# Optimization experiments

Hardware: AMD Instinct MI355X
Metric: run time of the kernel (lower is better)

The kernel has to match this reference:

```python
import jax, jax.numpy as jnp
import numpy as np

DIM = 32          # d_model == channel dim of the volume
D_STATE = 16
D_CONV = 4
EXPAND = 2
D_INNER = EXPAND * DIM        # 64
DT_RANK = max(1, (DIM + 15) // 16)  # ceil(d_model/16) = 2
LN_EPS = 1e-5


def setup_inputs() -> dict:
    key = jax.random.key(0)
    ks = jax.random.split(key, 12)
    B, Dd, Hh, Ww = 1, 32, 32, 32
    sc = 0.02
    x = jax.random.normal(ks[0], (B, DIM, Dd, Hh, Ww), jnp.float32)
    ln_w = jnp.ones((DIM,), jnp.float32)
    ln_b = jnp.zeros((DIM,), jnp.float32)
    in_proj_w = jax.random.normal(ks[1], (2 * D_INNER, DIM), jnp.float32) * sc
    conv_w = jax.random.normal(ks[2], (D_INNER, 1, D_CONV), jnp.float32) * sc
    conv_b = jnp.zeros((D_INNER,), jnp.float32)
    x_proj_w = jax.random.normal(ks[3], (DT_RANK + 2 * D_STATE, D_INNER), jnp.float32) * sc
    dt_proj_w = jax.random.normal(ks[4], (D_INNER, DT_RANK), jnp.float32) * sc
    dt_proj_b = jax.random.uniform(ks[5], (D_INNER,), jnp.float32, -4.0, -2.0)  # small softplus(dt) at init
    # Mamba S4D-real init: A = -[1..d_state], stored as A_log
    A_log = jnp.log(jnp.broadcast_to(jnp.arange(1, D_STATE + 1, dtype=jnp.float32), (D_INNER, D_STATE)))
    D_param = jnp.ones((D_INNER,), jnp.float32)
    out_proj_w = jax.random.normal(ks[6], (DIM, D_INNER), jnp.float32) * sc
    return {
        "x": x, "ln_w": ln_w, "ln_b": ln_b, "in_proj_w": in_proj_w,
        "conv_w": conv_w, "conv_b": conv_b, "x_proj_w": x_proj_w,
        "dt_proj_w": dt_proj_w, "dt_proj_b": dt_proj_b, "A_log": A_log,
        "D_param": D_param, "out_proj_w": out_proj_w,
    }


def _mamba_layer(x, ln_w, ln_b, in_proj_w, conv_w, conv_b, x_proj_w,
                 dt_proj_w, dt_proj_b, A_log, D_param, out_proj_w):
    B, C, Dd, Hh, Ww = x.shape
    L = Dd * Hh * Ww
    # z-scan flatten: (B, C, D, H, W) -> (B, L, C)
    xf = x.reshape(B, C, L).transpose(0, 2, 1)
    # LayerNorm over channel dim
    mu = jnp.mean(xf, axis=-1, keepdims=True)
    var = jnp.mean(jnp.square(xf - mu), axis=-1, keepdims=True)
    xn = (xf - mu) * jax.lax.rsqrt(var + LN_EPS) * ln_w + ln_b
    # in_proj -> x, z branches
    xz = xn @ in_proj_w.T                      # (B, L, 2*d_inner)
    x_in, z = jnp.split(xz, 2, axis=-1)
    # depthwise causal conv1d over sequence
    xt = x_in.transpose(0, 2, 1)               # (B, d_inner, L)
    xc = jax.lax.conv_general_dilated(
        xt, conv_w, window_strides=(1,), padding=[(D_CONV - 1, 0)],
        feature_group_count=D_INNER)
    xc = jax.nn.silu(xc + conv_b[None, :, None]).transpose(0, 2, 1)  # (B, L, d_inner)
    # input-dependent dt, B, C
    x_dbl = xc @ x_proj_w.T                    # (B, L, dt_rank + 2*d_state)
    dt, Bm, Cm = jnp.split(x_dbl, [DT_RANK, DT_RANK + D_STATE], axis=-1)
    delta = jax.nn.softplus(dt @ dt_proj_w.T + dt_proj_b)            # (B, L, d_inner)
    A = -jnp.exp(A_log)                        # (d_inner, d_state)
    # discretize: h_t = exp(delta*A) h_{t-1} + delta*B_t*x_t
    dA = jnp.exp(delta[..., None] * A)                               # (B, L, d_inner, d_state)
    dBx = delta[..., None] * Bm[:, :, None, :] * xc[..., None]       # (B, L, d_inner, d_state)
    def comb(e1, e2):
        a1, b1 = e1
        a2, b2 = e2
        return (a1 * a2, a2 * b1 + b2)
    _, h = jax.lax.associative_scan(comb, (dA, dBx), axis=1)         # parallel linear recurrence
    y = jnp.einsum('blds,bls->bld', h, Cm) + xc * D_param            # (B, L, d_inner)
    y = y * jax.nn.silu(z)
    out = y @ out_proj_w.T                     # (B, L, C)
    # unpermute z-scan
    return out.transpose(0, 2, 1).reshape(B, C, Dd, Hh, Ww)


def reference(x, ln_w, ln_b, in_proj_w, conv_w, conv_b, x_proj_w,
              dt_proj_w, dt_proj_b, A_log, D_param, out_proj_w):
    return _mamba_layer(x, ln_w, ln_b, in_proj_w, conv_w, conv_b, x_proj_w,
                        dt_proj_w, dt_proj_b, A_log, D_param, out_proj_w)
```

## Files before the change

### kernel.cpp

```cpp
#include <hip/hip_runtime.h>
#include <hip/hip_bf16.h>

constexpr int L   = 32768;
constexpr int CD  = 32;
constexpr int DI  = 64;
constexpr int DS  = 16;
constexpr int LC  = 64;
constexpr int NCH = L / LC;
constexpr int NPAIR = DI * DS;

constexpr size_t FL        = (size_t)DI * L;
constexpr size_t OFF_SZ    = 0;
constexpr size_t OFF_XC    = FL;
constexpr size_t OFF_DELTA = 2 * FL;
constexpr size_t OFF_BM    = 3 * FL;
constexpr size_t OFF_CM    = OFF_BM + (size_t)DS * L;
constexpr size_t OFF_APROD = OFF_CM + (size_t)DS * L;
constexpr size_t OFF_CARRY = OFF_APROD;
constexpr size_t OFF_BACC  = OFF_APROD + (size_t)NCH * NPAIR;

__device__ __forceinline__ float bf2f(__hip_bfloat16 v) { return __bfloat162float(v); }
__device__ __forceinline__ void f4arr(const float4 v, float* a) { a[0]=v.x; a[1]=v.y; a[2]=v.z; a[3]=v.w; }

__device__ __forceinline__ bool detect_bf16(const void* ln_w) {
    return ((const unsigned short*)ln_w)[0] == 0x3F80;
}
__device__ __forceinline__ float ldin(const void* p, size_t i, bool bf16) {
    return bf16 ? bf2f(((const __hip_bfloat16*)p)[i]) : ((const float*)p)[i];
}

__global__ __launch_bounds__(256) void k12_featurize_scan(
    const void* __restrict__ x,
    const void* __restrict__ ln_w,
    const void* __restrict__ ln_b,
    const void* __restrict__ in_proj_w,
    const void* __restrict__ conv_w,
    const void* __restrict__ conv_b,
    const void* __restrict__ x_proj_w,
    const void* __restrict__ dt_proj_w,
    const void* __restrict__ dt_proj_b,
    const void* __restrict__ A_log,
    float* __restrict__ ws)
{
    __shared__ __align__(16) char smem[67840];
    float (*xin_s)[69]  = (float(*)[69])(smem);
    char* AR = smem + 17664;
    float (*xn_s)[33]   = (float(*)[33])(AR);
    float (*w_in_s)[32] = (float(*)[32])(AR + 8848);
    float (*sdl)[68]    = (float(*)[68])(AR);
    float (*sxc)[68]    = (float(*)[68])(AR + 17408);
    float (*sbm)[68]    = (float(*)[68])(AR + 34816);
    char* FW = smem + 56832;
    float (*w_xp)[64]   = (float(*)[64])(FW);
    float (*w_cv)[4]    = (float(*)[4])(FW + 8704);
    float (*w_dt)[2]    = (float(*)[2])(FW + 9728);
    float* b_dt_s = (float*)(FW + 10240);
    float* b_cv_s = (float*)(FW + 10496);
    float* lnw_s  = (float*)(FW + 10752);
    float* lnb_s  = (float*)(FW + 10880);

    const int tid = threadIdx.x;
    const int l0  = blockIdx.x * LC;
    const bool isb = detect_bf16(ln_w);

    if (isb) {
        const __hip_bfloat16* ipw = (const __hip_bfloat16*)in_proj_w;
        const __hip_bfloat16* xpw = (const __hip_bfloat16*)x_proj_w;
        for (int i = tid; i < 128 * 32; i += 256) w_in_s[i >> 5][i & 31] = bf2f(ipw[i]);
        for (int i = tid; i < 34 * 64; i += 256)  w_xp[i >> 6][i & 63] = bf2f(xpw[i]);
    } else {
        const float* ipw = (const float*)in_proj_w;
        const float* xpw = (const float*)x_proj_w;
        for (int i = tid; i < 128 * 32; i += 256) w_in_s[i >> 5][i & 31] = ipw[i];
        for (int i = tid; i < 34 * 64; i += 256)  w_xp[i >> 6][i & 63] = xpw[i];
    }
    w_cv[tid >> 2][tid & 3] = ldin(conv_w, tid, isb);
    if (tid < 128) w_dt[tid >> 1][tid & 1] = ldin(dt_proj_w, tid, isb);
    if (tid < 64) { b_dt_s[tid] = ldin(dt_proj_b, tid, isb); b_cv_s[tid] = ldin(conv_b, tid, isb); }
    if (tid < 32) { lnw_s[tid] = ldin(ln_w, tid, isb); lnb_s[tid] = ldin(ln_b, tid, isb); }
    __syncthreads();

    if (tid < LC + 3) {
        const int l = l0 - 3 + tid;
        const bool valid = (l >= 0);
        const int lc = valid ? l : 0;
        float xv[CD];
        if (isb) {
            const __hip_bfloat16* xb = (const __hip_bfloat16*)x;
            #pragma unroll
            for (int c = 0; c < CD; ++c) xv[c] = bf2f(xb[(size_t)c * L + lc]);
        } else {
            const float* xf = (const float*)x;
            #pragma unroll
            for (int c = 0; c < CD; ++c) xv[c] = xf[(size_t)c * L + lc];
        }
        float mu = 0.f;
        #pragma unroll
        for (int c = 0; c < CD; ++c) mu += xv[c];
        mu *= (1.f / CD);
        float var = 0.f;
        #pragma unroll
        for (int c = 0; c < CD; ++c) { const float dc = xv[c] - mu; var += dc * dc; }
        const float rstd = rsqrtf(var * (1.f / CD) + 1e-5f);
        #pragma unroll
        for (int c = 0; c < CD; ++c)
            xn_s[tid][c] = valid ? ((xv[c] - mu) * rstd * lnw_s[c] + lnb_s[c]) : 0.f;
    }
    __syncthreads();

    {
        const int wv   = tid >> 6;
        const int lane = tid & 63;
        const int jb   = wv * 32;
        if (wv < 2) {
            const int pos1  = 64 + lane;
            const bool v1   = (pos1 < LC + 3);
            const int pos1c = v1 ? pos1 : 66;
            float xv0[CD], xv1[CD];
            #pragma unroll
            for (int c = 0; c < CD; ++c) { xv0[c] = xn_s[lane][c]; xv1[c] = xn_s[pos1c][c]; }
            for (int j = 0; j < 32; ++j) {
                const float4* wr = (const float4*)w_in_s[jb + j];
                float a0 = 0.f, a1 = 0.f;
                #pragma unroll
                for (int q = 0; q < 8; ++q) {
                    const float4 w4 = wr[q];
                    a0 += w4.x * xv0[4*q] + w4.y * xv0[4*q+1] + w4.z * xv0[4*q+2] + w4.w * xv0[4*q+3];
                    a1 += w4.x * xv1[4*q] + w4.y * xv1[4*q+1] + w4.z * xv1[4*q+2] + w4.w * xv1[4*q+3];
                }
                xin_s[jb + j][lane] = a0;
                if (v1) xin_s[jb + j][pos1] = a1;
            }
        } else {
            const int l = l0 + lane;
            float xv[CD];
            #pragma unroll
            for (int c = 0; c < CD; ++c) xv[c] = xn_s[3 + lane][c];
            for (int j = 0; j < 32; ++j) {
                const float4* wr = (const float4*)w_in_s[jb + j];
                float acc = 0.f;
                #pragma unroll
                for (int q = 0; q < 8; ++q) {
                    const float4 w4 = wr[q];
                    acc += w4.x * xv[4*q] + w4.y * xv[4*q+1] + w4.z * xv[4*q+2] + w4.w * xv[4*q+3];
                }
                const float s = acc / (1.f + __expf(-acc));
                ws[OFF_SZ + (size_t)(jb - 64 + j) * L + l] = s;
            }
        }
    }
    __syncthreads();

    {
        const int h  = tid & 3;
        const int pq = tid >> 2;
        const int l  = l0 + pq;
        const int dbase = h * 16;
        float xcv[16];
        #pragma unroll
        for (int i = 0; i < 16; ++i) {
            const int d = dbase + i;
            float acc = b_cv_s[d];
            #pragma unroll
            for (int k = 0; k < 4; ++k) acc += w_cv[d][k] * xin_s[d][pq + k];
            const float v = acc / (1.f + __expf(-acc));
            xcv[i] = v;
            ws[OFF_XC + (size_t)d * L + l] = v;
            sxc[d][pq] = v;
        }
        float dt0 = 0.f, dt1 = 0.f;
        for (int r = 0; r < 34; ++r) {
            float acc = 0.f;
            #pragma unroll
            for (int i = 0; i < 16; ++i) acc += w_xp[r][dbase + i] * xcv[i];
            acc += __shfl_xor(acc, 1);
            acc += __shfl_xor(acc, 2);
            if (r == 0) dt0 = acc;
            else if (r == 1) dt1 = acc;
            else {
                const int rr = r - 2;
                if (h == (rr >> 3)) {
                    const size_t off = (rr < 16) ? (OFF_BM + (size_t)rr * L)
                                                 : (OFF_CM + (size_t)(rr - 16) * L);
                    ws[off + l] = acc;
                    if (rr < 16) sbm[rr][pq] = acc;
                }
            }
        }
        #pragma unroll
        for (int i = 0; i < 16; ++i) {
            const int d = dbase + i;
            const float tv = dt0 * w_dt[d][0] + dt1 * w_dt[d][1] + b_dt_s[d];
            const float sp = fmaxf(tv, 0.f) + log1pf(__expf(-fabsf(tv)));
            ws[OFF_DELTA + (size_t)d * L + l] = sp;
            sdl[d][pq] = sp;
        }
    }
    __syncthreads();

    {
        const int d = tid >> 2, sg = tid & 3;
        float Aj[4], ap[4] = {1.f, 1.f, 1.f, 1.f}, bb[4] = {0.f, 0.f, 0.f, 0.f};
        #pragma unroll
        for (int j = 0; j < 4; ++j) Aj[j] = -__expf(ldin(A_log, d * DS + sg + 4 * j, isb));

        for (int t = 0; t < LC; t += 4) {
            float ddv[4], xxv[4], bm[4][4];
            f4arr(*(const float4*)&sdl[d][t], ddv);
            f4arr(*(const float4*)&sxc[d][t], xxv);
            f4arr(*(const float4*)&sbm[sg][t],      bm[0]);
            f4arr(*(const float4*)&sbm[sg + 4][t],  bm[1]);
            f4arr(*(const float4*)&sbm[sg + 8][t],  bm[2]);
            f4arr(*(const float4*)&sbm[sg + 12][t], bm[3]);
            #pragma unroll
            for (int tt = 0; tt < 4; ++tt) {
                const float dxc = ddv[tt] * xxv[tt];
                #pragma unroll
                for (int j = 0; j < 4; ++j) {
                    const float e = __expf(ddv[tt] * Aj[j]);
                    ap[j] *= e;
                    bb[j] = e * bb[j] + dxc * bm[j][tt];
                }
            }
        }
        #pragma unroll
        for (int j = 0; j < 4; ++j) {
            const size_t p = (size_t)(tid * 4 + j);
            ws[OFF_APROD + p * NCH + blockIdx.x] = ap[j];
            ws[OFF_BACC  + p * NCH + blockIdx.x] = bb[j];
        }
    }
}

__global__ __launch_bounds__(256) void k3_carry(float* __restrict__ ws)
{
    const int lane = threadIdx.x & 63;
    const int p    = blockIdx.x * 4 + (threadIdx.x >> 6);
    const size_t row_a = OFF_APROD + (size_t)p * NCH;
    const size_t row_b = OFF_BACC  + (size_t)p * NCH;

    float a[8], b[8];
    f4arr(*(const float4*)&ws[row_a + lane * 8],     a);
    f4arr(*(const float4*)&ws[row_a + lane * 8 + 4], a + 4);
    f4arr(*(const float4*)&ws[row_b + lane * 8],     b);
    f4arr(*(const float4*)&ws[row_b + lane * 8 + 4], b + 4);

    float Ag = a[0], Bg = b[0];
    #pragma unroll
    for (int i = 1; i < 8; ++i) { Bg = a[i] * Bg + b[i]; Ag = Ag * a[i]; }
    #pragma unroll
    for (int off = 1; off < 64; off <<= 1) {
        const float pa = __shfl_up(Ag, off);
        const float pb = __shfl_up(Bg, off);
        if (lane >= off) { Bg = Ag * pb + Bg; Ag = Ag * pa; }
    }
    float Pb = __shfl_up(Bg, 1);
    if (lane == 0) Pb = 0.f;
    float cr[8];
    #pragma unroll
    for (int i = 0; i < 8; ++i) { cr[i] = Pb; Pb = a[i] * Pb + b[i]; }
    *(float4*)&ws[OFF_CARRY + (size_t)p * NCH + lane * 8]     = make_float4(cr[0], cr[1], cr[2], cr[3]);
    *(float4*)&ws[OFF_CARRY + (size_t)p * NCH + lane * 8 + 4] = make_float4(cr[4], cr[5], cr[6], cr[7]);
}

__global__ __launch_bounds__(256, 3) void k45_apply_out(
    const void* __restrict__ A_log,
    const void* __restrict__ D_param,
    const void* __restrict__ ln_w,
    const void* __restrict__ out_proj_w,
    float* __restrict__ ws,
    void* __restrict__ out)
{
    __shared__ __align__(16) float sbm[DS][68];
    __shared__ __align__(16) float scm[DS][68];
    __shared__ __align__(16) float sy[DI][68];
    __shared__ float w_out_s[CD][DI];
    const int tid = threadIdx.x;
    const int c   = blockIdx.x;
    const size_t t0 = (size_t)c * LC;
    const bool isb = detect_bf16(ln_w);

    if (isb) {
        const __hip_bfloat16* opw = (const __hip_bfloat16*)out_proj_w;
        for (int i = tid; i < CD * DI; i += 256) w_out_s[i >> 6][i & 63] = bf2f(opw[i]);
    } else {
        const float* opw = (const float*)out_proj_w;
        for (int i = tid; i < CD * DI; i += 256) w_out_s[i >> 6][i & 63] = opw[i];
    }
    {
        const int r = tid >> 4, t4 = (tid & 15) * 4;
        *(float4*)&sbm[r][t4] = *(const float4*)&ws[OFF_BM + (size_t)r * L + t0 + t4];
        *(float4*)&scm[r][t4] = *(const float4*)&ws[OFF_CM + (size_t)r * L + t0 + t4];
    }

    const int d = tid >> 2, sg = tid & 3;
    float Aj[4];
    #pragma unroll
    for (int j = 0; j < 4; ++j) Aj[j] = -__expf(ldin(A_log, d * DS + sg + 4 * j, isb));
    const float Dd = ldin(D_param, d, isb);
    float hh[4];
    #pragma unroll
    for (int j = 0; j < 4; ++j) hh[j] = ws[OFF_CARRY + (size_t)(tid * 4 + j) * NCH + c];
    __syncthreads();

    const float* dlp = ws + OFF_DELTA + (size_t)d * L + t0;
    const float* xcp = ws + OFF_XC    + (size_t)d * L + t0;
    float4 dd4 = *(const float4*)dlp;
    float4 xx4 = *(const float4*)xcp;
    for (int t = 0; t < LC; t += 4) {
        const int tn = (t + 4) & 63;
        const float4 ddn = *(const float4*)(dlp + tn);
        const float4 xxn = *(const float4*)(xcp + tn);
        float ddv[4], xxv[4], bm[4][4], cm[4][4];
        f4arr(dd4, ddv);
        f4arr(xx4, xxv);
        f4arr(*(const float4*)&sbm[sg][t],      bm[0]);
        f4arr(*(const float4*)&sbm[sg + 4][t],  bm[1]);
        f4arr(*(const float4*)&sbm[sg + 8][t],  bm[2]);
        f4arr(*(const float4*)&sbm[sg + 12][t], bm[3]);
        f4arr(*(const float4*)&scm[sg][t],      cm[0]);
        f4arr(*(const float4*)&scm[sg + 4][t],  cm[1]);
        f4arr(*(const float4*)&scm[sg + 8][t],  cm[2]);
        f4arr(*(const float4*)&scm[sg + 12][t], cm[3]);
        #pragma unroll
        for (int tt = 0; tt < 4; ++tt) {
            const float dxc = ddv[tt] * xxv[tt];
            float ys = 0.f;
            #pragma unroll
            for (int j = 0; j < 4; ++j) {
                const float e = __expf(ddv[tt] * Aj[j]);
                hh[j] = e * hh[j] + dxc * bm[j][tt];
                ys += hh[j] * cm[j][tt];
            }
            ys += __shfl_xor(ys, 1);
            ys += __shfl_xor(ys, 2);
            if (sg == 0) sy[d][t + tt] = ys + xxv[tt] * Dd;
        }
        dd4 = ddn; xx4 = xxn;
    }
    __syncthreads();

    #pragma unroll
    for (int k = 0; k < 4; ++k) {
        const int idx = tid + k * 256;
        const int r = idx >> 4, t4 = (idx & 15) * 4;
        float4 yv = *(float4*)&sy[r][t4];
        const float4 zv = *(const float4*)&ws[OFF_SZ + (size_t)r * L + t0 + t4];
        yv.x *= zv.x; yv.y *= zv.y; yv.z *= zv.z; yv.w *= zv.w;
        *(float4*)&sy[r][t4] = yv;
    }
    __syncthreads();

    {
        const int wv   = tid >> 6;
        const int lane = tid & 63;
        float acc[8] = {0.f, 0.f, 0.f, 0.f, 0.f, 0.f, 0.f, 0.f};
        for (int dd = 0; dd < DI; ++dd) {
            const float yv = sy[dd][lane];
            #pragma unroll
            for (int j = 0; j < 8; ++j)
                acc[j] += yv * w_out_s[wv * 8 + j][dd];
        }
        const size_t l = t0 + lane;
        #pragma unroll
        for (int j = 0; j < 8; ++j) {
            const int cc = wv * 8 + j;
            if (isb) ((__hip_bfloat16*)out)[(size_t)cc * L + l] = __float2bfloat16(acc[j]);
            else     ((float*)out)[(size_t)cc * L + l] = acc[j];
        }
    }
}

extern "C" void kernel_launch(void* const* d_in, const int* in_sizes, int n_in,
                              void* d_out, int out_size, void* d_ws, size_t ws_size,
                              hipStream_t stream)
{
    (void)in_sizes; (void)n_in; (void)out_size; (void)ws_size;
    const void* x        = d_in[0];
    const void* ln_w     = d_in[1];
    const void* ln_b     = d_in[2];
    const void* in_pw    = d_in[3];
    const void* conv_w   = d_in[4];
    const void* conv_b   = d_in[5];
    const void* x_pw     = d_in[6];
    const void* dt_pw    = d_in[7];
    const void* dt_pb    = d_in[8];
    const void* A_log    = d_in[9];
    const void* D_param  = d_in[10];
    const void* out_pw   = d_in[11];
    float* ws = (float*)d_ws;

    k12_featurize_scan<<<NCH, 256, 0, stream>>>(x, ln_w, ln_b, in_pw, conv_w, conv_b,
                                                x_pw, dt_pw, dt_pb, A_log, ws);
    k3_carry<<<NPAIR / 4, 256, 0, stream>>>(ws);
    k45_apply_out<<<NCH, 256, 0, stream>>>(A_log, D_param, ln_w, out_pw, ws, d_out);
}
```

Baseline: 162.0 us.

## Fuse three-kernel Mamba pipeline into one cooperative kernel with grid syncs

```diff
diff --git a/kernel.cpp b/kernel.cpp
--- a/kernel.cpp
+++ b/kernel.cpp
@@ -1,5 +1,8 @@
 #include <hip/hip_runtime.h>
 #include <hip/hip_bf16.h>
+#include <hip/hip_cooperative_groups.h>
+
+namespace cg = cooperative_groups;
 
 constexpr int L   = 32768;
 constexpr int CD  = 32;
@@ -8,6 +11,10 @@
 constexpr int LC  = 64;
 constexpr int NCH = L / LC;
 constexpr int NPAIR = DI * DS;
+
+constexpr size_t COFF_A = 0;
+constexpr size_t COFF_B = (size_t)NCH * NPAIR;
+constexpr size_t COFF_C = 2 * (size_t)NCH * NPAIR;
 
 constexpr size_t FL        = (size_t)DI * L;
 constexpr size_t OFF_SZ    = 0;
@@ -27,6 +34,316 @@
 }
 __device__ __forceinline__ float ldin(const void* p, size_t i, bool bf16) {
     return bf16 ? bf2f(((const __hip_bfloat16*)p)[i]) : ((const float*)p)[i];
+}
+
+__global__ __launch_bounds__(256, 2) void mamba_fused(
+    const void* __restrict__ x,
+    const void* __restrict__ ln_w,
+    const void* __restrict__ ln_b,
+    const void* __restrict__ in_proj_w,
+    const void* __restrict__ conv_w,
+    const void* __restrict__ conv_b,
+    const void* __restrict__ x_proj_w,
+    const void* __restrict__ dt_proj_w,
+    const void* __restrict__ dt_proj_b,
+    const void* __restrict__ A_log,
+    const void* __restrict__ D_param,
+    const void* __restrict__ out_proj_w,
+    float* __restrict__ ws,
+    void* __restrict__ out)
+{
+    __shared__ __align__(16) char smem[72192];
+    float (*xin_s)[69]  = (float(*)[69])(smem);
+    float (*ctile)[512] = (float(*)[512])(smem);
+    float (*sy)[68]     = (float(*)[68])(smem);
+    char* AR = smem + 17664;
+    float (*xn_s)[33]   = (float(*)[33])(AR);
+    float (*w_in_s)[32] = (float(*)[32])(AR + 8848);
+    float (*sdl)[68]    = (float(*)[68])(AR);
+    float (*sxc)[68]    = (float(*)[68])(AR + 17408);
+    float (*sbm)[68]    = (float(*)[68])(AR + 34816);
+    float (*scm)[68]    = (float(*)[68])(AR + 39168);
+    char* FW = smem + 61184;
+    float (*w_xp)[64]   = (float(*)[64])(FW);
+    float (*w_out_s)[64]= (float(*)[64])(FW);
+    float (*w_cv)[4]    = (float(*)[4])(FW + 8704);
+    float (*w_dt)[2]    = (float(*)[2])(FW + 9728);
+    float* b_dt_s = (float*)(FW + 10240);
+    float* b_cv_s = (float*)(FW + 10496);
+    float* lnw_s  = (float*)(FW + 10752);
+    float* lnb_s  = (float*)(FW + 10880);
+
+    cg::grid_group grid = cg::this_grid();
+
+    const int tid  = threadIdx.x;
+    const int c    = blockIdx.x;
+    const int l0   = c * LC;
+    const int wv   = tid >> 6;
+    const int lane = tid & 63;
+    const bool isb = detect_bf16(ln_w);
+
+    float szr[32];
+    float Aj[4];
+
+    if (isb) {
+        const __hip_bfloat16* ipw = (const __hip_bfloat16*)in_proj_w;
+        const __hip_bfloat16* xpw = (const __hip_bfloat16*)x_proj_w;
+        for (int i = tid; i < 128 * 32; i += 256) w_in_s[i >> 5][i & 31] = bf2f(ipw[i]);
+        for (int i = tid; i < 34 * 64; i += 256)  w_xp[i >> 6][i & 63] = bf2f(xpw[i]);
+    } else {
+        const float* ipw = (const float*)in_proj_w;
+        const float* xpw = (const float*)x_proj_w;
+        for (int i = tid; i < 128 * 32; i += 256) w_in_s[i >> 5][i & 31] = ipw[i];
+        for (int i = tid; i < 34 * 64; i += 256)  w_xp[i >> 6][i & 63] = xpw[i];
+    }
+    w_cv[tid >> 2][tid & 3] = ldin(conv_w, tid, isb);
+    if (tid < 128) w_dt[tid >> 1][tid & 1] = ldin(dt_proj_w, tid, isb);
+    if (tid < 64) { b_dt_s[tid] = ldin(dt_proj_b, tid, isb); b_cv_s[tid] = ldin(conv_b, tid, isb); }
+    if (tid < 32) { lnw_s[tid] = ldin(ln_w, tid, isb); lnb_s[tid] = ldin(ln_b, tid, isb); }
+    __syncthreads();
+
+    if (tid < LC + 3) {
+        const int l = l0 - 3 + tid;
+        const bool valid = (l >= 0);
+        const int lc = valid ? l : 0;
+        float xv[CD];
+        if (isb) {
+            const __hip_bfloat16* xb = (const __hip_bfloat16*)x;
+            #pragma unroll
+            for (int ch = 0; ch < CD; ++ch) xv[ch] = bf2f(xb[(size_t)ch * L + lc]);
+        } else {
+            const float* xf = (const float*)x;
+            #pragma unroll
+            for (int ch = 0; ch < CD; ++ch) xv[ch] = xf[(size_t)ch * L + lc];
+        }
+        float mu = 0.f;
+        #pragma unroll
+        for (int ch = 0; ch < CD; ++ch) mu += xv[ch];
+        mu *= (1.f / CD);
+        float var = 0.f;
+        #pragma unroll
+        for (int ch = 0; ch < CD; ++ch) { const float dc = xv[ch] - mu; var += dc * dc; }
+        const float rstd = rsqrtf(var * (1.f / CD) + 1e-5f);
+        #pragma unroll
+        for (int ch = 0; ch < CD; ++ch)
+            xn_s[tid][ch] = valid ? ((xv[ch] - mu) * rstd * lnw_s[ch] + lnb_s[ch]) : 0.f;
+    }
+    __syncthreads();
+
+    if (wv < 2) {
+        const int jb = wv * 32;
+        const int pos1  = 64 + lane;
+        const bool v1   = (pos1 < LC + 3);
+        const int pos1c = v1 ? pos1 : 66;
+        float xv0[CD], xv1[CD];
+        #pragma unroll
+        for (int ch = 0; ch < CD; ++ch) { xv0[ch] = xn_s[lane][ch]; xv1[ch] = xn_s[pos1c][ch]; }
+        for (int j = 0; j < 32; ++j) {
+            const float4* wr = (const float4*)w_in_s[jb + j];
+            float a0 = 0.f, a1 = 0.f;
+            #pragma unroll
+            for (int q = 0; q < 8; ++q) {
+                const float4 w4 = wr[q];
+                a0 += w4.x * xv0[4*q] + w4.y * xv0[4*q+1] + w4.z * xv0[4*q+2] + w4.w * xv0[4*q+3];
+                a1 += w4.x * xv1[4*q] + w4.y * xv1[4*q+1] + w4.z * xv1[4*q+2] + w4.w * xv1[4*q+3];
+            }
+            xin_s[jb + j][lane] = a0;
+            if (v1) xin_s[jb + j][pos1] = a1;
+        }
+    } else {
+        const int jb = wv * 32;
+        float xv[CD];
+        #pragma unroll
+        for (int ch = 0; ch < CD; ++ch) xv[ch] = xn_s[3 + lane][ch];
+        #pragma unroll
+        for (int j = 0; j < 32; ++j) {
+            const float4* wr = (const float4*)w_in_s[jb + j];
+            float acc = 0.f;
+            #pragma unroll
+            for (int q = 0; q < 8; ++q) {
+                const float4 w4 = wr[q];
+                acc += w4.x * xv[4*q] + w4.y * xv[4*q+1] + w4.z * xv[4*q+2] + w4.w * xv[4*q+3];
+            }
+            szr[j] = acc / (1.f + __expf(-acc));
+        }
+    }
+    __syncthreads();
+
+    {
+        const int h  = tid & 3;
+        const int pq = tid >> 2;
+        const int dbase = h * 16;
+        float xcv[16];
+        #pragma unroll
+        for (int i = 0; i < 16; ++i) {
+            const int d = dbase + i;
+            float acc = b_cv_s[d];
+            #pragma unroll
+            for (int k = 0; k < 4; ++k) acc += w_cv[d][k] * xin_s[d][pq + k];
+            const float v = acc / (1.f + __expf(-acc));
+            xcv[i] = v;
+            sxc[d][pq] = v;
+        }
+        float dt0 = 0.f, dt1 = 0.f;
+        for (int r = 0; r < 34; ++r) {
+            float acc = 0.f;
+            #pragma unroll
+            for (int i = 0; i < 16; ++i) acc += w_xp[r][dbase + i] * xcv[i];
+            acc += __shfl_xor(acc, 1);
+            acc += __shfl_xor(acc, 2);
+            if (r == 0) dt0 = acc;
+            else if (r == 1) dt1 = acc;
+            else {
+                const int rr = r - 2;
+                if (h == (rr >> 3)) {
+                    if (rr < 16) sbm[rr][pq] = acc;
+                    else         scm[rr - 16][pq] = acc;
+                }
+            }
+        }
+        #pragma unroll
+        for (int i = 0; i < 16; ++i) {
+            const int d = dbase + i;
+            const float tv = dt0 * w_dt[d][0] + dt1 * w_dt[d][1] + b_dt_s[d];
+            const float sp = fmaxf(tv, 0.f) + log1pf(__expf(-fabsf(tv)));
+            sdl[d][pq] = sp;
+        }
+    }
+    __syncthreads();
+
+    if (isb) {
+        const __hip_bfloat16* opw = (const __hip_bfloat16*)out_proj_w;
+        for (int i = tid; i < CD * DI; i += 256) w_out_s[i >> 6][i & 63] = bf2f(opw[i]);
+    } else {
+        const float* opw = (const float*)out_proj_w;
+        for (int i = tid; i < CD * DI; i += 256) w_out_s[i >> 6][i & 63] = opw[i];
+    }
+
+    {
+        const int d = tid >> 2, sg = tid & 3;
+        float ap[4] = {1.f, 1.f, 1.f, 1.f}, bb[4] = {0.f, 0.f, 0.f, 0.f};
+        #pragma unroll
+        for (int j = 0; j < 4; ++j) Aj[j] = -__expf(ldin(A_log, d * DS + sg + 4 * j, isb));
+
+        for (int t = 0; t < LC; t += 4) {
+            float ddv[4], xxv[4], bm[4][4];
+            f4arr(*(const float4*)&sdl[d][t], ddv);
+            f4arr(*(const float4*)&sxc[d][t], xxv);
+            f4arr(*(const float4*)&sbm[sg][t],      bm[0]);
+            f4arr(*(const float4*)&sbm[sg + 4][t],  bm[1]);
+            f4arr(*(const float4*)&sbm[sg + 8][t],  bm[2]);
+            f4arr(*(const float4*)&sbm[sg + 12][t], bm[3]);
+            #pragma unroll
+            for (int tt = 0; tt < 4; ++tt) {
+                const float dxc = ddv[tt] * xxv[tt];
+                #pragma unroll
+                for (int j = 0; j < 4; ++j) {
+                    const float e = __expf(ddv[tt] * Aj[j]);
+                    ap[j] *= e;
+                    bb[j] = e * bb[j] + dxc * bm[j][tt];
+                }
+            }
+        }
+        *(float4*)&ws[COFF_A + (size_t)c * NPAIR + tid * 4] = make_float4(ap[0], ap[1], ap[2], ap[3]);
+        *(float4*)&ws[COFF_B + (size_t)c * NPAIR + tid * 4] = make_float4(bb[0], bb[1], bb[2], bb[3]);
+    }
+    __threadfence();
+    grid.sync();
+
+    if (c < NPAIR / 4) {
+        const int p = c * 4 + wv;
+        float a[8], b[8];
+        #pragma unroll
+        for (int i = 0; i < 8; ++i) {
+            const size_t ch = (size_t)(lane * 8 + i);
+            a[i] = ws[COFF_A + ch * NPAIR + p];
+            b[i] = ws[COFF_B + ch * NPAIR + p];
+        }
+        float Ag = a[0], Bg = b[0];
+        #pragma unroll
+        for (int i = 1; i < 8; ++i) { Bg = a[i] * Bg + b[i]; Ag = Ag * a[i]; }
+        #pragma unroll
+        for (int off = 1; off < 64; off <<= 1) {
+            const float pa = __shfl_up(Ag, off);
+            const float pb = __shfl_up(Bg, off);
+            if (lane >= off) { Bg = Ag * pb + Bg; Ag = Ag * pa; }
+        }
+        float Pb = __shfl_up(Bg, 1);
+        if (lane == 0) Pb = 0.f;
+        #pragma unroll
+        for (int i = 0; i < 8; ++i) { ctile[wv][lane * 8 + i] = Pb; Pb = a[i] * Pb + b[i]; }
+        __syncthreads();
+        #pragma unroll
+        for (int r = 0; r < 2; ++r) {
+            const int ch = tid + 256 * r;
+            *(float4*)&ws[COFF_C + (size_t)ch * NPAIR + c * 4] =
+                make_float4(ctile[0][ch], ctile[1][ch], ctile[2][ch], ctile[3][ch]);
+        }
+    }
+    __threadfence();
+    grid.sync();
+
+    {
+        const int d = tid >> 2, sg = tid & 3;
+        const float Dd = ldin(D_param, d, isb);
+        float hh[4];
+        {
+            const float4 h4 = *(const float4*)&ws[COFF_C + (size_t)c * NPAIR + tid * 4];
+            hh[0] = h4.x; hh[1] = h4.y; hh[2] = h4.z; hh[3] = h4.w;
+        }
+        for (int t = 0; t < LC; t += 4) {
+            float ddv[4], xxv[4], bm[4][4], cm[4][4];
+            f4arr(*(const float4*)&sdl[d][t], ddv);
+            f4arr(*(const float4*)&sxc[d][t], xxv);
+            f4arr(*(const float4*)&sbm[sg][t],      bm[0]);
+            f4arr(*(const float4*)&sbm[sg + 4][t],  bm[1]);
+            f4arr(*(const float4*)&sbm[sg + 8][t],  bm[2]);
+            f4arr(*(const float4*)&sbm[sg + 12][t], bm[3]);
+            f4arr(*(const float4*)&scm[sg][t],      cm[0]);
+            f4arr(*(const float4*)&scm[sg + 4][t],  cm[1]);
+            f4arr(*(const float4*)&scm[sg + 8][t],  cm[2]);
+            f4arr(*(const float4*)&scm[sg + 12][t], cm[3]);
+            #pragma unroll
+            for (int tt = 0; tt < 4; ++tt) {
+                const float dxc = ddv[tt] * xxv[tt];
+                float ys = 0.f;
+                #pragma unroll
+                for (int j = 0; j < 4; ++j) {
+                    const float e = __expf(ddv[tt] * Aj[j]);
+                    hh[j] = e * hh[j] + dxc * bm[j][tt];
+                    ys += hh[j] * cm[j][tt];
+                }
+                ys += __shfl_xor(ys, 1);
+                ys += __shfl_xor(ys, 2);
+                if (sg == 0) sy[d][t + tt] = ys + xxv[tt] * Dd;
+            }
+        }
+    }
+    __syncthreads();
+
+    if (wv >= 2) {
+        const int rbase = (wv - 2) * 32;
+        #pragma unroll
+        for (int j = 0; j < 32; ++j) sy[rbase + j][lane] *= szr[j];
+    }
+    __syncthreads();
+
+    {
+        float acc[8] = {0.f, 0.f, 0.f, 0.f, 0.f, 0.f, 0.f, 0.f};
+        for (int dd = 0; dd < DI; ++dd) {
+            const float yv = sy[dd][lane];
+            #pragma unroll
+            for (int j = 0; j < 8; ++j)
+                acc[j] += yv * w_out_s[wv * 8 + j][dd];
+        }
+        const size_t l = (size_t)l0 + lane;
+        #pragma unroll
+        for (int j = 0; j < 8; ++j) {
+            const int cc = wv * 8 + j;
+            if (isb) ((__hip_bfloat16*)out)[(size_t)cc * L + l] = __float2bfloat16(acc[j]);
+            else     ((float*)out)[(size_t)cc * L + l] = acc[j];
+        }
+    }
 }
 
 __global__ __launch_bounds__(256) void k12_featurize_scan(
@@ -389,6 +706,20 @@
     const void* D_param  = d_in[10];
     const void* out_pw   = d_in[11];
     float* ws = (float*)d_ws;
+    void* o   = d_out;
+
+    static int use_coop = -1;
+    if (use_coop != 0) {
+        void* kargs[] = { (void*)&x, (void*)&ln_w, (void*)&ln_b, (void*)&in_pw,
+                          (void*)&conv_w, (void*)&conv_b, (void*)&x_pw, (void*)&dt_pw,
+                          (void*)&dt_pb, (void*)&A_log, (void*)&D_param, (void*)&out_pw,
+                          (void*)&ws, (void*)&o };
+        const hipError_t e = hipLaunchCooperativeKernel(
+            reinterpret_cast<const void*>(&mamba_fused),
+            dim3(NCH), dim3(256), kargs, 0u, stream);
+        if (e == hipSuccess) { use_coop = 1; return; }
+        use_coop = 0;
+    }
 
     k12_featurize_scan<<<NCH, 256, 0, stream>>>(x, ln_w, ln_b, in_pw, conv_w, conv_b,
                                                 x_pw, dt_pw, dt_pb, A_log, ws);
```

After: 161.0 us. About the same (-0.6%).

## Shrink shared memory via aliasing and transpose chunk-carry layout for coalescing

Applied to the files above, without the earlier changes.

```diff
diff --git a/kernel.cpp b/kernel.cpp
--- a/kernel.cpp
+++ b/kernel.cpp
@@ -29,7 +29,24 @@
     return bf16 ? bf2f(((const __hip_bfloat16*)p)[i]) : ((const float*)p)[i];
 }
 
-__global__ __launch_bounds__(256) void k12_featurize_scan(
+__device__ __forceinline__ float dot32_g(const void* w, int row, const float* xv, bool isb) {
+    float acc = 0.f;
+    if (isb) {
+        const __hip_bfloat16* p = (const __hip_bfloat16*)w + (size_t)row * 32;
+        #pragma unroll
+        for (int c = 0; c < 32; ++c) acc += bf2f(p[c]) * xv[c];
+    } else {
+        const float4* p = (const float4*)((const float*)w + (size_t)row * 32);
+        #pragma unroll
+        for (int q = 0; q < 8; ++q) {
+            const float4 w4 = p[q];
+            acc += w4.x * xv[4*q] + w4.y * xv[4*q+1] + w4.z * xv[4*q+2] + w4.w * xv[4*q+3];
+        }
+    }
+    return acc;
+}
+
+__global__ __launch_bounds__(256, 3) void k12_featurize_scan(
     const void* __restrict__ x,
     const void* __restrict__ ln_w,
     const void* __restrict__ ln_b,
@@ -42,15 +59,15 @@
     const void* __restrict__ A_log,
     float* __restrict__ ws)
 {
-    __shared__ __align__(16) char smem[67840];
-    float (*xin_s)[69]  = (float(*)[69])(smem);
-    char* AR = smem + 17664;
+    __shared__ __align__(16) char smem[53648];
+    float (*xin_s)[68]  = (float(*)[68])(smem);
+    float (*sxc)[68]    = (float(*)[68])(smem);
+    char* AR = smem + 17408;
     float (*xn_s)[33]   = (float(*)[33])(AR);
     float (*w_in_s)[32] = (float(*)[32])(AR + 8848);
     float (*sdl)[68]    = (float(*)[68])(AR);
-    float (*sxc)[68]    = (float(*)[68])(AR + 17408);
-    float (*sbm)[68]    = (float(*)[68])(AR + 34816);
-    char* FW = smem + 56832;
+    float (*sbm)[68]    = (float(*)[68])(AR + 17408);
+    char* FW = smem + 42640;
     float (*w_xp)[64]   = (float(*)[64])(FW);
     float (*w_cv)[4]    = (float(*)[4])(FW + 8704);
     float (*w_dt)[2]    = (float(*)[2])(FW + 9728);
@@ -113,23 +130,18 @@
         const int lane = tid & 63;
         const int jb   = wv * 32;
         if (wv < 2) {
-            const int pos1  = 64 + lane;
-            const bool v1   = (pos1 < LC + 3);
-            const int pos1c = v1 ? pos1 : 66;
-            float xv0[CD], xv1[CD];
-            #pragma unroll
-            for (int c = 0; c < CD; ++c) { xv0[c] = xn_s[lane][c]; xv1[c] = xn_s[pos1c][c]; }
+            float xv0[CD];
+            #pragma unroll
+            for (int c = 0; c < CD; ++c) xv0[c] = xn_s[lane][c];
             for (int j = 0; j < 32; ++j) {
                 const float4* wr = (const float4*)w_in_s[jb + j];
-                float a0 = 0.f, a1 = 0.f;
+                float a0 = 0.f;
                 #pragma unroll
                 for (int q = 0; q < 8; ++q) {
                     const float4 w4 = wr[q];
                     a0 += w4.x * xv0[4*q] + w4.y * xv0[4*q+1] + w4.z * xv0[4*q+2] + w4.w * xv0[4*q+3];
-                    a1 += w4.x * xv1[4*q] + w4.y * xv1[4*q+1] + w4.z * xv1[4*q+2] + w4.w * xv1[4*q+3];
                 }
                 xin_s[jb + j][lane] = a0;
-                if (v1) xin_s[jb + j][pos1] = a1;
             }
         } else {
             const int l = l0 + lane;
@@ -147,6 +159,18 @@
                 const float s = acc / (1.f + __expf(-acc));
                 ws[OFF_SZ + (size_t)(jb - 64 + j) * L + l] = s;
             }
+            {
+                const int col0 = (wv == 2) ? 64 : 65;
+                float xvh[CD];
+                #pragma unroll
+                for (int c = 0; c < CD; ++c) xvh[c] = xn_s[col0][c];
+                xin_s[lane][col0] = dot32_g(in_proj_w, lane, xvh, isb);
+                if (wv == 3) {
+                    #pragma unroll
+                    for (int c = 0; c < CD; ++c) xvh[c] = xn_s[66][c];
+                    xin_s[lane][66] = dot32_g(in_proj_w, lane, xvh, isb);
+                }
+            }
         }
     }
     __syncthreads();
@@ -166,7 +190,6 @@
             const float v = acc / (1.f + __expf(-acc));
             xcv[i] = v;
             ws[OFF_XC + (size_t)d * L + l] = v;
-            sxc[d][pq] = v;
         }
         float dt0 = 0.f, dt1 = 0.f;
         for (int r = 0; r < 34; ++r) {
@@ -195,6 +218,9 @@
             ws[OFF_DELTA + (size_t)d * L + l] = sp;
             sdl[d][pq] = sp;
         }
+        __syncthreads();
+        #pragma unroll
+        for (int i = 0; i < 16; ++i) sxc[dbase + i][pq] = xcv[i];
     }
     __syncthreads();
 
@@ -223,27 +249,25 @@
                 }
             }
         }
-        #pragma unroll
-        for (int j = 0; j < 4; ++j) {
-            const size_t p = (size_t)(tid * 4 + j);
-            ws[OFF_APROD + p * NCH + blockIdx.x] = ap[j];
-            ws[OFF_BACC  + p * NCH + blockIdx.x] = bb[j];
-        }
+        *(float4*)&ws[OFF_APROD + (size_t)blockIdx.x * NPAIR + tid * 4] = make_float4(ap[0], ap[1], ap[2], ap[3]);
+        *(float4*)&ws[OFF_BACC  + (size_t)blockIdx.x * NPAIR + tid * 4] = make_float4(bb[0], bb[1], bb[2], bb[3]);
     }
 }
 
 __global__ __launch_bounds__(256) void k3_carry(float* __restrict__ ws)
 {
+    __shared__ float ctile[4][512];
     const int lane = threadIdx.x & 63;
-    const int p    = blockIdx.x * 4 + (threadIdx.x >> 6);
-    const size_t row_a = OFF_APROD + (size_t)p * NCH;
-    const size_t row_b = OFF_BACC  + (size_t)p * NCH;
+    const int wv   = threadIdx.x >> 6;
+    const int p    = blockIdx.x * 4 + wv;
 
     float a[8], b[8];
-    f4arr(*(const float4*)&ws[row_a + lane * 8],     a);
-    f4arr(*(const float4*)&ws[row_a + lane * 8 + 4], a + 4);
-    f4arr(*(const float4*)&ws[row_b + lane * 8],     b);
-    f4arr(*(const float4*)&ws[row_b + lane * 8 + 4], b + 4);
+    #pragma unroll
+    for (int i = 0; i < 8; ++i) {
+        const size_t ch = (size_t)(lane * 8 + i);
+        a[i] = ws[OFF_APROD + ch * NPAIR + p];
+        b[i] = ws[OFF_BACC  + ch * NPAIR + p];
+    }
 
     float Ag = a[0], Bg = b[0];
     #pragma unroll
@@ -256,14 +280,18 @@
     }
     float Pb = __shfl_up(Bg, 1);
     if (lane == 0) Pb = 0.f;
-    float cr[8];
-    #pragma unroll
-    for (int i = 0; i < 8; ++i) { cr[i] = Pb; Pb = a[i] * Pb + b[i]; }
-    *(float4*)&ws[OFF_CARRY + (size_t)p * NCH + lane * 8]     = make_float4(cr[0], cr[1], cr[2], cr[3]);
-    *(float4*)&ws[OFF_CARRY + (size_t)p * NCH + lane * 8 + 4] = make_float4(cr[4], cr[5], cr[6], cr[7]);
-}
-
-__global__ __launch_bounds__(256, 3) void k45_apply_out(
+    #pragma unroll
+    for (int i = 0; i < 8; ++i) { ctile[wv][lane * 8 + i] = Pb; Pb = a[i] * Pb + b[i]; }
+    __syncthreads();
+    #pragma unroll
+    for (int r = 0; r < 2; ++r) {
+        const int ch = threadIdx.x + 256 * r;
+        *(float4*)&ws[OFF_CARRY + (size_t)ch * NPAIR + blockIdx.x * 4] =
+            make_float4(ctile[0][ch], ctile[1][ch], ctile[2][ch], ctile[3][ch]);
+    }
+}
+
+__global__ __launch_bounds__(256, 4) void k45_apply_out(
     const void* __restrict__ A_log,
     const void* __restrict__ D_param,
     const void* __restrict__ ln_w,
@@ -271,22 +299,17 @@
     float* __restrict__ ws,
     void* __restrict__ out)
 {
-    __shared__ __align__(16) float sbm[DS][68];
-    __shared__ __align__(16) float scm[DS][68];
-    __shared__ __align__(16) float sy[DI][68];
-    __shared__ float w_out_s[CD][DI];
+    __shared__ __align__(16) char smem45[26112];
+    float (*sy)[68]      = (float(*)[68])(smem45);
+    float (*sbm)[68]     = (float(*)[68])(smem45 + 17408);
+    float (*scm)[68]     = (float(*)[68])(smem45 + 21760);
+    float (*w_out_s)[64] = (float(*)[64])(smem45 + 17408);
+
     const int tid = threadIdx.x;
     const int c   = blockIdx.x;
     const size_t t0 = (size_t)c * LC;
     const bool isb = detect_bf16(ln_w);
 
-    if (isb) {
-        const __hip_bfloat16* opw = (const __hip_bfloat16*)out_proj_w;
-        for (int i = tid; i < CD * DI; i += 256) w_out_s[i >> 6][i & 63] = bf2f(opw[i]);
-    } else {
-        const float* opw = (const float*)out_proj_w;
-        for (int i = tid; i < CD * DI; i += 256) w_out_s[i >> 6][i & 63] = opw[i];
-    }
     {
         const int r = tid >> 4, t4 = (tid & 15) * 4;
         *(float4*)&sbm[r][t4] = *(const float4*)&ws[OFF_BM + (size_t)r * L + t0 + t4];
@@ -299,8 +322,10 @@
     for (int j = 0; j < 4; ++j) Aj[j] = -__expf(ldin(A_log, d * DS + sg + 4 * j, isb));
     const float Dd = ldin(D_param, d, isb);
     float hh[4];
-    #pragma unroll
-    for (int j = 0; j < 4; ++j) hh[j] = ws[OFF_CARRY + (size_t)(tid * 4 + j) * NCH + c];
+    {
+        const float4 h4 = *(const float4*)&ws[OFF_CARRY + (size_t)c * NPAIR + tid * 4];
+        hh[0] = h4.x; hh[1] = h4.y; hh[2] = h4.z; hh[3] = h4.w;
+    }
     __syncthreads();
 
     const float* dlp = ws + OFF_DELTA + (size_t)d * L + t0;
@@ -340,6 +365,14 @@
     }
     __syncthreads();
 
+    if (isb) {
+        const __hip_bfloat16* opw = (const __hip_bfloat16*)out_proj_w;
+        for (int i = tid; i < CD * DI; i += 256) w_out_s[i >> 6][i & 63] = bf2f(opw[i]);
+    } else {
+        const float* opw = (const float*)out_proj_w;
+        for (int i = tid; i < CD * DI; i += 256) w_out_s[i >> 6][i & 63] = opw[i];
+    }
+
     #pragma unroll
     for (int k = 0; k < 4; ++k) {
         const int idx = tid + k * 256;
```

New measurement: 154.7 us. -4.5%, faster.
